# Optimization experiments

Hardware: AMD Instinct MI355X
Metric: run time of the kernel (lower is better)

Reference implementation:

```python
import jax, jax.numpy as jnp
import numpy as np

N, E, D, ED, FD, H, Q, K, G = 50000, 600000, 128, 128, 512, 1, 3, 512, 512
NEG_SLOPE = 0.2
EPS = 1e-5


def setup_inputs() -> dict:
    key = jax.random.key(0)
    ks = jax.random.split(key, 16)
    inp = {
        'x': jax.random.normal(ks[0], (N, D), jnp.float32),
        'edge_index': jax.random.randint(ks[1], (2, E), 0, N, jnp.int32),
        'edge_attr': jax.random.normal(ks[2], (E, ED), jnp.float32),
        'batch_vec': jnp.sort(jax.random.randint(ks[3], (N,), 0, G, jnp.int32)),
        'W_l': jax.random.normal(ks[4], (D, H * D), jnp.float32),
        'b_l': jnp.zeros((H * D,), jnp.float32),
        'W_r': jax.random.normal(ks[5], (D, H * D), jnp.float32),
        'b_r': jnp.zeros((H * D,), jnp.float32),
        'W_edge': jax.random.normal(ks[6], (ED, H * D), jnp.float32),
        'att': jax.random.normal(ks[7], (H, D), jnp.float32),
        'conv_bias': jnp.zeros((H * D,), jnp.float32),
        'adapter_W': jax.random.normal(ks[8], (D, D), jnp.float32),
        'adapter_b': jnp.zeros((D,), jnp.float32),
        'norm_g': jnp.ones((D,), jnp.float32),
        'norm_b': jnp.zeros((D,), jnp.float32),
        'codebooks': jax.random.normal(ks[9], (Q, K, D), jnp.float32),
        'out_W': jax.random.normal(ks[10], (D, FD), jnp.float32),
        'out_b': jnp.zeros((FD,), jnp.float32),
        'outnorm_g': jnp.ones((FD,), jnp.float32),
        'outnorm_b': jnp.zeros((FD,), jnp.float32),
    }
    return inp


def _layer_norm(x, g, b):
    m = x.mean(-1, keepdims=True)
    v = ((x - m) ** 2).mean(-1, keepdims=True)
    return (x - m) * jax.lax.rsqrt(v + EPS) * g + b


def _forward(x, edge_index, edge_attr, batch_vec, W_l, b_l, W_r, b_r, W_edge, att,
             conv_bias, adapter_W, adapter_b, norm_g, norm_b, codebooks, out_W, out_b,
             outnorm_g, outnorm_b):
    sg = jax.lax.stop_gradient
    n = x.shape[0]
    # ---- GATv2Conv (PyG defaults: add_self_loops=True, fill_value='mean') ----
    loops = jnp.arange(n, dtype=edge_index.dtype)
    src = jnp.concatenate([edge_index[0], loops])
    dst = jnp.concatenate([edge_index[1], loops])
    mean_attr = edge_attr.mean(0)
    ea = jnp.concatenate([edge_attr, jnp.broadcast_to(mean_attr, (n, edge_attr.shape[1]))])
    xl = (x @ W_l + b_l).reshape(n, H, D)   # source transform
    xr = (x @ W_r + b_r).reshape(n, H, D)   # target transform
    e_emb = (ea @ W_edge).reshape(-1, H, D)
    e = xl[src] + xr[dst] + e_emb           # [Etot,H,D]
    score = jnp.einsum('ehd,hd->eh', jax.nn.leaky_relu(e, NEG_SLOPE), att)
    smax = jax.ops.segment_max(score, dst, num_segments=n)
    ex = jnp.exp(score - smax[dst])
    denom = jax.ops.segment_sum(ex, dst, num_segments=n)
    alpha = ex / (denom[dst] + 1e-16)       # per-target softmax
    out = jax.ops.segment_sum(xl[src] * alpha[..., None], dst, num_segments=n)  # [n,H,D]
    out = out.reshape(n, H * D) + conv_bias
    h = out.reshape(n, H, D).mean(1)        # mean over heads
    # ---- global mean pool over graphs ----
    sums = jax.ops.segment_sum(h, batch_vec, num_segments=G)
    cnts = jax.ops.segment_sum(jnp.ones((n,), h.dtype), batch_vec, num_segments=G)
    g = sums / jnp.maximum(cnts, 1.0)[:, None]
    # ---- adapter + layernorm ----
    g = g @ adapter_W + adapter_b
    g = _layer_norm(g, norm_g, norm_b)
    # ---- residual VQ (euclidean nearest code, straight-through) ----
    residual = g
    quantized_out = jnp.zeros_like(g)
    codes, idxs, commits = [], [], []
    cb_sq = (codebooks ** 2).sum(-1)        # [Q,K]
    for q in range(Q):
        cb = codebooks[q]
        d2 = (residual ** 2).sum(-1, keepdims=True) - 2.0 * residual @ cb.T + cb_sq[q]
        idx = jnp.argmin(d2, axis=-1)
        code = cb[idx]
        commits.append(((sg(code) - residual) ** 2).mean())
        quantized_out = quantized_out + residual + sg(code - residual)
        codes.append(code)
        idxs.append(idx)
        residual = residual - sg(code)
    commit_loss = jnp.stack(commits).mean()
    residual_loss = ((g - quantized_out) ** 2).mean()
    loss = commit_loss + residual_loss
    indices = jnp.stack(idxs, axis=1)       # [G,Q]
    # ---- per-quantizer straight-through tokens -> projection -> layernorm ----
    tokens = jnp.stack([g + sg(c - g) for c in codes], axis=1)  # [G,Q,D]
    tokens = tokens @ out_W + out_b                              # [G,Q,FD]
    tokens = _layer_norm(tokens, outnorm_g, outnorm_b)
    return tokens, indices, loss


def reference(x, edge_index, edge_attr, batch_vec, W_l, b_l, W_r, b_r, W_edge, att,
              conv_bias, adapter_W, adapter_b, norm_g, norm_b, codebooks, out_W, out_b,
              outnorm_g, outnorm_b):
    return _forward(x, edge_index, edge_attr, batch_vec, W_l, b_l, W_r, b_r, W_edge,
                    att, conv_bias, adapter_W, adapter_b, norm_g, norm_b, codebooks,
                    out_W, out_b, outnorm_g, outnorm_b)
```

## Files before the change

### kernel.cpp

```cpp
#include <hip/hip_runtime.h>
#include <math.h>

#define N_NODES 50000
#define E_EDGES 600000
#define DD 128
#define G_GRAPHS 512
#define K_CODES 512
#define Q_QUANT 3
#define FD_OUT 512
#define NEG_SLOPE 0.2f
#define LN_EPS 1e-5f

using short8 = __attribute__((ext_vector_type(8))) short;
using f32x4  = __attribute__((ext_vector_type(4))) float;

static __device__ __forceinline__ float lrelu(float v){ return v > 0.f ? v : NEG_SLOPE*v; }
static __device__ __forceinline__ float wsum(float v){
#pragma unroll
  for (int m = 1; m < 64; m <<= 1) v += __shfl_xor(v, m);
  return v;
}
static __device__ __forceinline__ float wmax(float v){
#pragma unroll
  for (int m = 1; m < 64; m <<= 1) v = fmaxf(v, __shfl_xor(v, m));
  return v;
}
static __device__ __forceinline__ ushort f2bf(float f){
  unsigned u = __float_as_uint(f);
  unsigned r = (u + 0x7fffu + ((u >> 16) & 1u)) >> 16;
  return (ushort)r;
}
static __device__ __forceinline__ float bf2f(ushort s){
  return __uint_as_float(((unsigned)s) << 16);
}

#define EA_LD 130

__global__ __launch_bounds__(256)
void k_xform2(const float* __restrict__ x,
              const float* __restrict__ W_l, const float* __restrict__ b_l,
              const float* __restrict__ W_r, const float* __restrict__ b_r,
              float* __restrict__ xl, float* __restrict__ xr, int n)
{
  __shared__ __align__(16) float xt[64*EA_LD];
  __shared__ __align__(16) float WtL[32*128];
  __shared__ __align__(16) float WtR[32*128];
  const int tid = threadIdx.x;
  const int r0 = blockIdx.x * 64;
  {
    const int q = tid & 63, eb = tid >> 6;
#pragma unroll
    for (int i = 0; i < 16; ++i){
      int e = eb + 4*i;
      int row = r0 + e;
      float2 v = make_float2(0.f, 0.f);
      if (row < n) v = *(const float2*)&x[row*DD + q*2];
      *(float2*)&xt[e*EA_LD + q*2] = v;
    }
  }
  const int eg = tid >> 4;
  const int cg = tid & 15;
  float accL[4][8], accR[4][8];
#pragma unroll
  for (int j = 0; j < 4; ++j)
#pragma unroll
    for (int u = 0; u < 8; ++u){ accL[j][u] = 0.f; accR[j][u] = 0.f; }

  for (int kq = 0; kq < 4; ++kq){
    __syncthreads();
    {
      const int c4 = tid & 31, kb = tid >> 5;
#pragma unroll
      for (int i = 0; i < 4; ++i){
        int kk = kb + 8*i;
        *(float4*)&WtL[kk*128 + c4*4] = *(const float4*)&W_l[(kq*32+kk)*DD + c4*4];
        *(float4*)&WtR[kk*128 + c4*4] = *(const float4*)&W_r[(kq*32+kk)*DD + c4*4];
      }
    }
    __syncthreads();
    const int kb2 = kq*32;
#pragma unroll 4
    for (int k = 0; k < 32; ++k){
      float aa[4];
#pragma unroll
      for (int j = 0; j < 4; ++j) aa[j] = xt[(eg*4+j)*EA_LD + kb2 + k];
      float bL[8], bR[8];
      *(float4*)&bL[0] = *(const float4*)&WtL[k*128 + cg*4];
      *(float4*)&bL[4] = *(const float4*)&WtL[k*128 + 64 + cg*4];
      *(float4*)&bR[0] = *(const float4*)&WtR[k*128 + cg*4];
      *(float4*)&bR[4] = *(const float4*)&WtR[k*128 + 64 + cg*4];
#pragma unroll
      for (int j = 0; j < 4; ++j){
#pragma unroll
        for (int u = 0; u < 8; ++u) accL[j][u] = fmaf(aa[j], bL[u], accL[j][u]);
#pragma unroll
        for (int u = 0; u < 8; ++u) accR[j][u] = fmaf(aa[j], bR[u], accR[j][u]);
      }
    }
  }
  float bvL[8], bvR[8];
  *(float4*)&bvL[0] = *(const float4*)&b_l[cg*4];
  *(float4*)&bvL[4] = *(const float4*)&b_l[64 + cg*4];
  *(float4*)&bvR[0] = *(const float4*)&b_r[cg*4];
  *(float4*)&bvR[4] = *(const float4*)&b_r[64 + cg*4];
#pragma unroll
  for (int j = 0; j < 4; ++j){
    int row = r0 + eg*4 + j;
    if (row < n){
      float oL[8], oR[8];
#pragma unroll
      for (int u = 0; u < 8; ++u){ oL[u] = accL[j][u] + bvL[u]; oR[u] = accR[j][u] + bvR[u]; }
      *(float4*)&xl[row*DD + cg*4]      = *(const float4*)&oL[0];
      *(float4*)&xl[row*DD + 64 + cg*4] = *(const float4*)&oL[4];
      *(float4*)&xr[row*DD + cg*4]      = *(const float4*)&oR[0];
      *(float4*)&xr[row*DD + 64 + cg*4] = *(const float4*)&oR[4];
    }
  }
}

__global__ __launch_bounds__(128)
void k_wsplit(const float* __restrict__ W, ushort* __restrict__ Wbh, ushort* __restrict__ Wbl)
{
  const int n = blockIdx.x;
  const int k = threadIdx.x;
  float v = W[k*DD + n];
  ushort h = f2bf(v);
  Wbh[n*DD + k] = h;
  Wbl[n*DD + k] = f2bf(v - bf2f(h));
}

#define AP 40
#define WP 40
#define XSP 132

__global__ __launch_bounds__(256)
void k_edge(const float* __restrict__ edge_attr,
            const ushort* __restrict__ Wbh, const ushort* __restrict__ Wbl,
            const int* __restrict__ ei, const float* __restrict__ xl,
            const float* __restrict__ xr, const float* __restrict__ att,
            const int* __restrict__ off, int* __restrict__ pos,
            uint2* __restrict__ rec, float* __restrict__ asum_mid)
{
  __shared__ __align__(16) char smem[64*XSP*4];
  ushort* Ah = (ushort*)smem;
  ushort* Al = (ushort*)(smem + 5120);
  ushort* Wh = (ushort*)(smem + 10240);
  ushort* Wl = (ushort*)(smem + 20480);
  float*  xs = (float*)smem;

  const int tid = threadIdx.x;
  const int w = tid >> 6, lane = tid & 63;
  const int e0 = blockIdx.x * 64;

  const int ar  = tid & 63;
  const int ak  = w * 8;
  const int wn  = tid & 127;
  const int wk2 = (tid >> 7) * 16;

  const int mrow = w * 16 + (lane & 15);
  const int koff = (lane >> 4) * 8;
  const int nrow = lane & 15;

  f32x4 acc[8];
#pragma unroll
  for (int nt = 0; nt < 8; ++nt){ f32x4 z = {0.f,0.f,0.f,0.f}; acc[nt] = z; }

  for (int kq = 0; kq < 4; ++kq){
    if (kq) __syncthreads();
    float av[8];
    *(float4*)&av[0] = *(const float4*)&edge_attr[(size_t)(e0+ar)*DD + kq*32 + ak];
    *(float4*)&av[4] = *(const float4*)&edge_attr[(size_t)(e0+ar)*DD + kq*32 + ak + 4];
    short8 vh, vl;
#pragma unroll
    for (int i = 0; i < 8; ++i){
      ushort h = f2bf(av[i]);
      vh[i] = (short)h;
      vl[i] = (short)f2bf(av[i] - bf2f(h));
    }
    *(short8*)&Ah[ar*AP + ak] = vh;
    *(short8*)&Al[ar*AP + ak] = vl;
    {
      float cs[8];
#pragma unroll
      for (int i = 0; i < 8; ++i) cs[i] = av[i];
#pragma unroll
      for (int m = 1; m < 64; m <<= 1){
#pragma unroll
        for (int i = 0; i < 8; ++i) cs[i] += __shfl_xor(cs[i], m);
      }
      if (lane == 0){
#pragma unroll
        for (int i = 0; i < 8; ++i)
          atomicAdd(&asum_mid[(blockIdx.x & 63)*DD + kq*32 + ak + i], cs[i]);
      }
    }
    {
      const ushort* gh = &Wbh[wn*DD + kq*32 + wk2];
      const ushort* gl = &Wbl[wn*DD + kq*32 + wk2];
      *(short8*)&Wh[wn*WP + wk2]     = *(const short8*)&gh[0];
      *(short8*)&Wh[wn*WP + wk2 + 8] = *(const short8*)&gh[8];
      *(short8*)&Wl[wn*WP + wk2]     = *(const short8*)&gl[0];
      *(short8*)&Wl[wn*WP + wk2 + 8] = *(const short8*)&gl[8];
    }
    __syncthreads();
    short8 a_h = *(const short8*)&Ah[mrow*AP + koff];
    short8 a_l = *(const short8*)&Al[mrow*AP + koff];
    short8 bh[8];
#pragma unroll
    for (int nt = 0; nt < 8; ++nt)
      bh[nt] = *(const short8*)&Wh[(nt*16 + nrow)*WP + koff];
#pragma unroll
    for (int nt = 0; nt < 8; ++nt)
      acc[nt] = __builtin_amdgcn_mfma_f32_16x16x32_bf16(a_h, bh[nt], acc[nt], 0, 0, 0);
#pragma unroll
    for (int nt = 0; nt < 8; ++nt){
      short8 bl = *(const short8*)&Wl[(nt*16 + nrow)*WP + koff];
      acc[nt] = __builtin_amdgcn_mfma_f32_16x16x32_bf16(a_h, bl, acc[nt], 0, 0, 0);
    }
#pragma unroll
    for (int nt = 0; nt < 8; ++nt)
      acc[nt] = __builtin_amdgcn_mfma_f32_16x16x32_bf16(a_l, bh[nt], acc[nt], 0, 0, 0);
  }
  __syncthreads();
  {
    const int s0 = ei[e0 + ar];
    const int d0 = ei[E_EDGES + e0 + ar];
    const int cc = w * 32;
#pragma unroll
    for (int i = 0; i < 8; ++i){
      float4 a = *(const float4*)&xl[(size_t)s0*DD + cc + i*4];
      float4 b = *(const float4*)&xr[(size_t)d0*DD + cc + i*4];
      *(float4*)&xs[ar*XSP + cc + i*4] = make_float4(a.x+b.x, a.y+b.y, a.z+b.z, a.w+b.w);
    }
  }
  __syncthreads();
  float attv[8];
#pragma unroll
  for (int nt = 0; nt < 8; ++nt) attv[nt] = att[nt*16 + nrow];
  float p[4] = {0.f, 0.f, 0.f, 0.f};
  const int rb = w*16 + (lane >> 4)*4;
#pragma unroll
  for (int nt = 0; nt < 8; ++nt){
#pragma unroll
    for (int j = 0; j < 4; ++j){
      float ev = acc[nt][j] + xs[(rb + j)*XSP + nt*16 + nrow];
      p[j] += lrelu(ev) * attv[nt];
    }
  }
#pragma unroll
  for (int m = 1; m < 16; m <<= 1){
#pragma unroll
    for (int j = 0; j < 4; ++j) p[j] += __shfl_xor(p[j], m);
  }
  if ((lane & 15) == 0){
#pragma unroll
    for (int j = 0; j < 4; ++j){
      int e = e0 + rb + j;
      int d = ei[E_EDGES + e];
      int s = ei[e];
      int pp = atomicAdd(&pos[d], 1);
      uint2 r; r.x = (unsigned)s; r.y = __float_as_uint(p[j]);
      rec[off[d] + pp] = r;
    }
  }
}

__global__ __launch_bounds__(128)
void k_me(const float* __restrict__ asum_mid, const float* __restrict__ W_edge,
          float* __restrict__ me)
{
  __shared__ float mean[128];
  const int d = threadIdx.x;
  float s = 0.f;
  for (int r = 0; r < 64; ++r) s += asum_mid[r*DD + d];
  mean[d] = s / (float)E_EDGES;
  __syncthreads();
  float acc = 0.f;
  for (int k = 0; k < 128; ++k) acc += mean[k] * W_edge[k*DD + d];
  me[d] = acc;
}

__global__ __launch_bounds__(256)
void k_hist(const int* __restrict__ ei, int* __restrict__ indeg)
{
  int e = blockIdx.x*256 + threadIdx.x;
  if (e < E_EDGES) atomicAdd(&indeg[ei[E_EDGES + e]], 1);
}

#define SC_NB ((N_NODES + 511) / 512)
__global__ __launch_bounds__(512)
void k_scan1(const int* __restrict__ indeg, int* __restrict__ off, int* __restrict__ bsum)
{
  __shared__ int s[512];
  const int tid = threadIdx.x;
  const int gid = blockIdx.x*512 + tid;
  int v = (gid < N_NODES) ? indeg[gid] : 0;
  s[tid] = v;
  __syncthreads();
  for (int d = 1; d < 512; d <<= 1){
    int t = (tid >= d) ? s[tid-d] : 0;
    __syncthreads();
    s[tid] += t;
    __syncthreads();
  }
  if (gid < N_NODES) off[gid] = s[tid] - v;
  if (tid == 511) bsum[blockIdx.x] = s[511];
}

__global__ __launch_bounds__(128)
void k_scan2(const int* __restrict__ bsum, int* __restrict__ boff)
{
  __shared__ int s[128];
  const int tid = threadIdx.x;
  int v = (tid < SC_NB) ? bsum[tid] : 0;
  s[tid] = v;
  __syncthreads();
  for (int d = 1; d < 128; d <<= 1){
    int t = (tid >= d) ? s[tid-d] : 0;
    __syncthreads();
    s[tid] += t;
    __syncthreads();
  }
  if (tid < SC_NB) boff[tid] = s[tid] - v;
}

__global__ __launch_bounds__(512)
void k_scan3(int* __restrict__ off, const int* __restrict__ boff)
{
  const int gid = blockIdx.x*512 + threadIdx.x;
  if (gid < N_NODES) off[gid] += boff[blockIdx.x];
  if (gid == 0) off[N_NODES] = E_EDGES;
}

__global__ __launch_bounds__(256)
void k_aggregate(const int* __restrict__ off, const uint2* __restrict__ rec,
                 const float* __restrict__ xl, const float* __restrict__ xr,
                 const float* __restrict__ me, const float* __restrict__ att,
                 const float* __restrict__ conv_bias, const int* __restrict__ batch_vec,
                 float* __restrict__ gsum, float* __restrict__ gcnt)
{
  __shared__ float hshare[4][128];
  __shared__ int bsh[4];
  const int tid = threadIdx.x, lane = tid & 63, wid = tid >> 6;
  const int i = blockIdx.x*4 + wid;
  float2 xli = *(const float2*)&xl[i*DD + lane*2];
  float2 xri = *(const float2*)&xr[i*DD + lane*2];
  float2 mev = *(const float2*)&me[lane*2];
  float2 attv = *(const float2*)&att[lane*2];
  float v0 = xli.x + xri.x + mev.x;
  float v1 = xli.y + xri.y + mev.y;
  float s_self = wsum(lrelu(v0)*attv.x + lrelu(v1)*attv.y);
  const int o0 = off[i], o1 = off[i+1];
  const int deg = o1 - o0;
  uint2 myrec = make_uint2(0u, __float_as_uint(-INFINITY));
  float m = s_self;
  if (lane < deg) myrec = rec[o0 + lane];
  m = fmaxf(m, __uint_as_float(myrec.y));
  for (int b = 64; b < deg; b += 64){
    int j = b + lane;
    if (j < deg) m = fmaxf(m, __uint_as_float(rec[o0 + j].y));
  }
  m = wmax(m);
  float wse = __expf(s_self - m);
  float den = wse;
  float a0 = wse * xli.x, a1 = wse * xli.y;
  if (deg <= 64){
    float msc = __uint_as_float(myrec.y);
    int msrc = (int)myrec.x;
#pragma unroll 4
    for (int j = 0; j < deg; ++j){
      float sc = __shfl(msc, j);
      int s = __shfl(msrc, j);
      float w = __expf(sc - m);
      den += w;
      float2 xs = *(const float2*)&xl[s*DD + lane*2];
      a0 = fmaf(w, xs.x, a0);
      a1 = fmaf(w, xs.y, a1);
    }
  } else {
#pragma unroll 4
    for (int j = 0; j < deg; ++j){
      uint2 r = rec[o0 + j];
      float w = __expf(__uint_as_float(r.y) - m);
      den += w;
      float2 xs = *(const float2*)&xl[(int)r.x*DD + lane*2];
      a0 = fmaf(w, xs.x, a0);
      a1 = fmaf(w, xs.y, a1);
    }
  }
  float inv = 1.0f / (den + 1e-16f);
  float2 cb2 = *(const float2*)&conv_bias[lane*2];
  float h0 = a0*inv + cb2.x;
  float h1 = a1*inv + cb2.y;
  int b = batch_vec[i];
  hshare[wid][lane*2]     = h0;
  hshare[wid][lane*2 + 1] = h1;
  if (lane == 0) bsh[wid] = b;
  __syncthreads();
  bool uni = (bsh[0]==bsh[1]) && (bsh[1]==bsh[2]) && (bsh[2]==bsh[3]);
  if (uni){
    if (wid == 0){
      float s0 = hshare[0][lane*2] + hshare[1][lane*2] + hshare[2][lane*2] + hshare[3][lane*2];
      float s1 = hshare[0][lane*2+1] + hshare[1][lane*2+1] + hshare[2][lane*2+1] + hshare[3][lane*2+1];
      atomicAdd(&gsum[b*DD + lane*2],     s0);
      atomicAdd(&gsum[b*DD + lane*2 + 1], s1);
      if (lane == 0) atomicAdd(&gcnt[b], 4.0f);
    }
  } else {
    atomicAdd(&gsum[b*DD + lane*2],     h0);
    atomicAdd(&gsum[b*DD + lane*2 + 1], h1);
    if (lane == 0) atomicAdd(&gcnt[b], 1.0f);
  }
}

__global__ __launch_bounds__(128)
void k_pool(const float* __restrict__ gsum, const float* __restrict__ gcnt,
            const float* __restrict__ aW, const float* __restrict__ ab,
            const float* __restrict__ ng, const float* __restrict__ nb,
            float* __restrict__ g_ln)
{
  __shared__ float row[128];
  __shared__ float red[128];
  const int g = blockIdx.x, d = threadIdx.x;
  float denom = fmaxf(gcnt[g], 1.0f);
  row[d] = gsum[g*DD + d] / denom;
  __syncthreads();
  double accd = (double)ab[d];
  for (int k = 0; k < 128; ++k) accd += (double)row[k] * (double)aW[k*DD + d];
  float a = (float)accd;
  red[d] = a; __syncthreads();
  for (int s = 64; s > 0; s >>= 1){ if (d < s) red[d] += red[d+s]; __syncthreads(); }
  float mean = red[0] / 128.f; __syncthreads();
  float c = a - mean;
  red[d] = c*c; __syncthreads();
  for (int s = 64; s > 0; s >>= 1){ if (d < s) red[d] += red[d+s]; __syncthreads(); }
  float var = red[0] / 128.f; __syncthreads();
  float inv = (float)(1.0 / sqrt((double)var + (double)LN_EPS));
  g_ln[g*DD + d] = c * inv * ng[d] + nb[d];
}

__global__ __launch_bounds__(256)
void k_rvq(const float* __restrict__ g_ln, const float* __restrict__ codebooks,
           float* __restrict__ ind_out, int* __restrict__ idx_i,
           float* __restrict__ accs)
{
  __shared__ __align__(16) float r_lds[128];
  __shared__ float red[128];
  __shared__ double bd[64];
  __shared__ int bi[64];
  __shared__ int chosen;
  const int g = blockIdx.x, tid = threadIdx.x;
  if (tid < 128) r_lds[tid] = g_ln[g*DD + tid];
  __syncthreads();
  const int cl = tid >> 2, dq = tid & 3;
  for (int q = 0; q < Q_QUANT; ++q){
    const float* cb = codebooks + (size_t)q * K_CODES * DD;
    double bestd = 1e300; int besti = 1 << 30;
    for (int r = 0; r < 8; ++r){
      int c = r*64 + cl;
      double rc = 0.0, cc = 0.0;
      const float4* cp = (const float4*)&cb[c*DD + dq*32];
      const float4* rp = (const float4*)&r_lds[dq*32];
#pragma unroll
      for (int i = 0; i < 8; ++i){
        float4 cv = cp[i]; float4 rv = rp[i];
        rc += (double)cv.x*rv.x + (double)cv.y*rv.y + (double)cv.z*rv.z + (double)cv.w*rv.w;
        cc += (double)cv.x*cv.x + (double)cv.y*cv.y + (double)cv.z*cv.z + (double)cv.w*cv.w;
      }
      rc += __shfl_xor(rc, 1); rc += __shfl_xor(rc, 2);
      cc += __shfl_xor(cc, 1); cc += __shfl_xor(cc, 2);
      if (dq == 0){
        double d2 = cc - 2.0*rc;
        if (d2 < bestd || (d2 == bestd && c < besti)){ bestd = d2; besti = c; }
      }
    }
    if (dq == 0){ bd[cl] = bestd; bi[cl] = besti; }
    __syncthreads();
    if (tid < 64){
      double d2 = bd[tid]; int ii = bi[tid];
#pragma unroll
      for (int m = 1; m < 64; m <<= 1){
        double od = __shfl_xor(d2, m); int oi = __shfl_xor(ii, m);
        if (od < d2 || (od == d2 && oi < ii)){ d2 = od; ii = oi; }
      }
      if (tid == 0) chosen = ii;
    }
    __syncthreads();
    const int idx = chosen;
    if (tid == 0){
      ind_out[g*Q_QUANT + q] = (float)idx;
      idx_i[g*Q_QUANT + q] = idx;
    }
    if (tid < 128){
      float cd = cb[idx*DD + tid];
      float diff = cd - r_lds[tid];
      red[tid] = diff * diff;
      r_lds[tid] -= cd;
    }
    __syncthreads();
    for (int s = 64; s > 0; s >>= 1){ if (tid < s) red[tid] += red[tid+s]; __syncthreads(); }
    if (tid == 0) atomicAdd(&accs[q], red[0]);
    __syncthreads();
  }
  if (tid < 128) red[tid] = r_lds[tid]*r_lds[tid];
  __syncthreads();
  for (int s = 64; s > 0; s >>= 1){ if (tid < s) red[tid] += red[tid+s]; __syncthreads(); }
  if (tid == 0) atomicAdd(&accs[3], red[0]);
}

__global__ __launch_bounds__(256)
void k_tokens(const float* __restrict__ codebooks, const int* __restrict__ idx_i,
              const float* __restrict__ out_W, const float* __restrict__ out_b,
              const float* __restrict__ og, const float* __restrict__ ob,
              float* __restrict__ tokens)
{
  __shared__ __align__(16) float c_lds[128];
  __shared__ float red[256];
  const int blk = blockIdx.x;
  const int g = blk / 3, q = blk % 3;
  const int tid = threadIdx.x;
  const int idx = idx_i[g*Q_QUANT + q];
  if (tid < 128) c_lds[tid] = codebooks[((size_t)q*K_CODES + idx)*DD + tid];
  __syncthreads();
  double v0 = (double)out_b[tid];
  double v1 = (double)out_b[tid + 256];
  for (int k = 0; k < 128; ++k){
    double ck = (double)c_lds[k];
    v0 += ck * (double)out_W[k*FD_OUT + tid];
    v1 += ck * (double)out_W[k*FD_OUT + tid + 256];
  }
  float f0 = (float)v0, f1 = (float)v1;
  red[tid] = f0 + f1; __syncthreads();
  for (int s = 128; s > 0; s >>= 1){ if (tid < s) red[tid] += red[tid+s]; __syncthreads(); }
  float mean = red[0] / 512.f; __syncthreads();
  float d0 = f0 - mean, d1 = f1 - mean;
  red[tid] = d0*d0 + d1*d1; __syncthreads();
  for (int s = 128; s > 0; s >>= 1){ if (tid < s) red[tid] += red[tid+s]; __syncthreads(); }
  float var = red[0] / 512.f; __syncthreads();
  float inv = (float)(1.0 / sqrt((double)var + (double)LN_EPS));
  tokens[(size_t)blk*FD_OUT + tid]       = d0*inv*og[tid] + ob[tid];
  tokens[(size_t)blk*FD_OUT + tid + 256] = d1*inv*og[tid+256] + ob[tid+256];
}

__global__ void k_loss(const float* __restrict__ accs, float* __restrict__ out)
{
  float commit = (accs[0] + accs[1] + accs[2]) / (3.0f * G_GRAPHS * DD);
  float resid  = accs[3] / ((float)G_GRAPHS * DD);
  out[0] = commit + resid;
}

extern "C" void kernel_launch(void* const* d_in, const int* in_sizes, int n_in,
                              void* d_out, int out_size, void* d_ws, size_t ws_size,
                              hipStream_t stream)
{
  (void)in_sizes; (void)n_in; (void)out_size; (void)ws_size;
  const float* x         = (const float*)d_in[0];
  const int*   ei        = (const int*)d_in[1];
  const float* edge_attr = (const float*)d_in[2];
  const int*   batch_vec = (const int*)d_in[3];
  const float* W_l       = (const float*)d_in[4];
  const float* b_l       = (const float*)d_in[5];
  const float* W_r       = (const float*)d_in[6];
  const float* b_r       = (const float*)d_in[7];
  const float* W_edge    = (const float*)d_in[8];
  const float* att       = (const float*)d_in[9];
  const float* conv_bias = (const float*)d_in[10];
  const float* aW        = (const float*)d_in[11];
  const float* ab        = (const float*)d_in[12];
  const float* ng        = (const float*)d_in[13];
  const float* nb        = (const float*)d_in[14];
  const float* codebooks = (const float*)d_in[15];
  const float* out_W     = (const float*)d_in[16];
  const float* out_b     = (const float*)d_in[17];
  const float* og        = (const float*)d_in[18];
  const float* ob        = (const float*)d_in[19];
  float* outf = (float*)d_out;

  char* w = (char*)d_ws;
  size_t o = 0;
  auto nxt = [&](size_t bytes)->void*{
    void* p = w + o;
    o += (bytes + 511) & ~(size_t)511;
    return p;
  };
  int*   indeg    = (int*)  nxt((size_t)N_NODES*4);
  int*   pos      = (int*)  nxt((size_t)N_NODES*4);
  float* asum_mid = (float*)nxt((size_t)64*DD*4);
  float* gsum     = (float*)nxt((size_t)G_GRAPHS*DD*4);
  float* gcnt     = (float*)nxt((size_t)G_GRAPHS*4);
  float* accs     = (float*)nxt(16);
  const size_t zero_span = o;
  int*   off      = (int*)  nxt((size_t)(N_NODES+1)*4);
  float* xl       = (float*)nxt((size_t)N_NODES*DD*4);
  float* xr       = (float*)nxt((size_t)N_NODES*DD*4);
  uint2* rec      = (uint2*)nxt((size_t)E_EDGES*8);
  float* me       = (float*)nxt((size_t)DD*4);
  float* g_ln     = (float*)nxt((size_t)G_GRAPHS*DD*4);
  int*   idx_i    = (int*)  nxt((size_t)G_GRAPHS*Q_QUANT*4);
  int*   bsum     = (int*)  nxt((size_t)SC_NB*4);
  int*   boff     = (int*)  nxt((size_t)SC_NB*4);
  ushort* Wbh     = (ushort*)nxt((size_t)DD*DD*2);
  ushort* Wbl     = (ushort*)nxt((size_t)DD*DD*2);

  hipMemsetAsync(w, 0, zero_span, stream);

  k_wsplit<<<dim3(128), dim3(128), 0, stream>>>(W_edge, Wbh, Wbl);
  k_hist<<<dim3((E_EDGES+255)/256), dim3(256), 0, stream>>>(ei, indeg);
  k_scan1<<<dim3(SC_NB), dim3(512), 0, stream>>>(indeg, off, bsum);
  k_scan2<<<dim3(1), dim3(128), 0, stream>>>(bsum, boff);
  k_scan3<<<dim3(SC_NB), dim3(512), 0, stream>>>(off, boff);
  k_xform2<<<dim3((N_NODES+63)/64), dim3(256), 0, stream>>>(x, W_l, b_l, W_r, b_r,
                                                            xl, xr, N_NODES);
  k_edge<<<dim3(E_EDGES/64), dim3(256), 0, stream>>>(edge_attr, Wbh, Wbl, ei, xl, xr, att,
                                                     off, pos, rec, asum_mid);
  k_me<<<dim3(1), dim3(128), 0, stream>>>(asum_mid, W_edge, me);
  k_aggregate<<<dim3(N_NODES/4), dim3(256), 0, stream>>>(off, rec, xl, xr, me, att,
                                                         conv_bias, batch_vec, gsum, gcnt);
  k_pool<<<dim3(G_GRAPHS), dim3(128), 0, stream>>>(gsum, gcnt, aW, ab, ng, nb, g_ln);
  k_rvq<<<dim3(G_GRAPHS), dim3(256), 0, stream>>>(g_ln, codebooks,
                                                  outf + (size_t)G_GRAPHS*Q_QUANT*FD_OUT,
                                                  idx_i, accs);
  k_tokens<<<dim3(G_GRAPHS*Q_QUANT), dim3(256), 0, stream>>>(codebooks, idx_i, out_W, out_b,
                                                             og, ob, outf);
  k_loss<<<dim3(1), dim3(1), 0, stream>>>(accs,
                                          outf + (size_t)G_GRAPHS*Q_QUANT*FD_OUT
                                               + (size_t)G_GRAPHS*Q_QUANT);
}
```

Baseline: 606.8 us.

## Keep W_edge fragments in registers and split edge GEMM by N across waves

The edge kernel no longer stages W_edge in shared memory per K-chunk. Each wave now loads its two 16-column slices of the split-bf16 weights straight into registers once, and the whole 64x128 edge_attr tile is converted and staged in LDS up front. This removes three of the four per-chunk barriers and the repeated weight LDS traffic. Because waves now partition columns instead of rows, per-wave attention partial sums are combined through a small LDS buffer, and a single thread per edge does the final atomic scatter. The cost is more registers for weight fragments and accumulators, and a larger LDS footprint that may lower occupancy.

```diff
diff --git a/kernel.cpp b/kernel.cpp
--- a/kernel.cpp
+++ b/kernel.cpp
@@ -129,8 +129,7 @@
   Wbl[n*DD + k] = f2bf(v - bf2f(h));
 }
 
-#define AP 40
-#define WP 40
+#define APS 136
 #define XSP 132
 
 __global__ __launch_bounds__(256)
@@ -141,127 +140,142 @@
             const int* __restrict__ off, int* __restrict__ pos,
             uint2* __restrict__ rec, float* __restrict__ asum_mid)
 {
-  __shared__ __align__(16) char smem[64*XSP*4];
+  __shared__ __align__(16) char smem[34816];
   ushort* Ah = (ushort*)smem;
-  ushort* Al = (ushort*)(smem + 5120);
-  ushort* Wh = (ushort*)(smem + 10240);
-  ushort* Wl = (ushort*)(smem + 20480);
+  ushort* Al = (ushort*)(smem + 17408);
   float*  xs = (float*)smem;
+  float*  ps = (float*)(smem + 33792);
 
   const int tid = threadIdx.x;
   const int w = tid >> 6, lane = tid & 63;
+  const int g = lane >> 4, f = lane & 15;
   const int e0 = blockIdx.x * 64;
-
-  const int ar  = tid & 63;
-  const int ak  = w * 8;
-  const int wn  = tid & 127;
-  const int wk2 = (tid >> 7) * 16;
-
-  const int mrow = w * 16 + (lane & 15);
-  const int koff = (lane >> 4) * 8;
-  const int nrow = lane & 15;
-
-  f32x4 acc[8];
-#pragma unroll
-  for (int nt = 0; nt < 8; ++nt){ f32x4 z = {0.f,0.f,0.f,0.f}; acc[nt] = z; }
-
+  const int koff = g * 8;
+  const int nt0 = w * 2;
+
+  short8 whF[2][4], wlF[2][4];
+#pragma unroll
+  for (int t = 0; t < 2; ++t){
+    const ushort* gh = &Wbh[((nt0+t)*16 + f)*DD];
+    const ushort* gl = &Wbl[((nt0+t)*16 + f)*DD];
+#pragma unroll
+    for (int kq = 0; kq < 4; ++kq){
+      whF[t][kq] = *(const short8*)&gh[kq*32 + koff];
+      wlF[t][kq] = *(const short8*)&gl[kq*32 + koff];
+    }
+  }
+
+  {
+    const int r = lane;
+    const int kc = w * 32;
+#pragma unroll
+    for (int c = 0; c < 4; ++c){
+      float av[8];
+      *(float4*)&av[0] = *(const float4*)&edge_attr[(size_t)(e0+r)*DD + kc + c*8];
+      *(float4*)&av[4] = *(const float4*)&edge_attr[(size_t)(e0+r)*DD + kc + c*8 + 4];
+      short8 vh, vl;
+#pragma unroll
+      for (int i = 0; i < 8; ++i){
+        ushort h = f2bf(av[i]);
+        vh[i] = (short)h;
+        vl[i] = (short)f2bf(av[i] - bf2f(h));
+      }
+      *(short8*)&Ah[r*APS + kc + c*8] = vh;
+      *(short8*)&Al[r*APS + kc + c*8] = vl;
+      float cs[8];
+#pragma unroll
+      for (int i = 0; i < 8; ++i) cs[i] = av[i];
+#pragma unroll
+      for (int m = 1; m < 64; m <<= 1){
+#pragma unroll
+        for (int i = 0; i < 8; ++i) cs[i] += __shfl_xor(cs[i], m);
+      }
+      if (lane == 0){
+#pragma unroll
+        for (int i = 0; i < 8; ++i)
+          atomicAdd(&asum_mid[(blockIdx.x & 63)*DD + kc + c*8 + i], cs[i]);
+      }
+    }
+  }
+  __syncthreads();
+
+  f32x4 acc[4][2];
+#pragma unroll
+  for (int m = 0; m < 4; ++m)
+#pragma unroll
+    for (int t = 0; t < 2; ++t){ f32x4 z = {0.f,0.f,0.f,0.f}; acc[m][t] = z; }
+
+#pragma unroll
   for (int kq = 0; kq < 4; ++kq){
-    if (kq) __syncthreads();
-    float av[8];
-    *(float4*)&av[0] = *(const float4*)&edge_attr[(size_t)(e0+ar)*DD + kq*32 + ak];
-    *(float4*)&av[4] = *(const float4*)&edge_attr[(size_t)(e0+ar)*DD + kq*32 + ak + 4];
-    short8 vh, vl;
-#pragma unroll
-    for (int i = 0; i < 8; ++i){
-      ushort h = f2bf(av[i]);
-      vh[i] = (short)h;
-      vl[i] = (short)f2bf(av[i] - bf2f(h));
-    }
-    *(short8*)&Ah[ar*AP + ak] = vh;
-    *(short8*)&Al[ar*AP + ak] = vl;
-    {
-      float cs[8];
-#pragma unroll
-      for (int i = 0; i < 8; ++i) cs[i] = av[i];
-#pragma unroll
-      for (int m = 1; m < 64; m <<= 1){
-#pragma unroll
-        for (int i = 0; i < 8; ++i) cs[i] += __shfl_xor(cs[i], m);
-      }
-      if (lane == 0){
-#pragma unroll
-        for (int i = 0; i < 8; ++i)
-          atomicAdd(&asum_mid[(blockIdx.x & 63)*DD + kq*32 + ak + i], cs[i]);
-      }
-    }
-    {
-      const ushort* gh = &Wbh[wn*DD + kq*32 + wk2];
-      const ushort* gl = &Wbl[wn*DD + kq*32 + wk2];
-      *(short8*)&Wh[wn*WP + wk2]     = *(const short8*)&gh[0];
-      *(short8*)&Wh[wn*WP + wk2 + 8] = *(const short8*)&gh[8];
-      *(short8*)&Wl[wn*WP + wk2]     = *(const short8*)&gl[0];
-      *(short8*)&Wl[wn*WP + wk2 + 8] = *(const short8*)&gl[8];
-    }
-    __syncthreads();
-    short8 a_h = *(const short8*)&Ah[mrow*AP + koff];
-    short8 a_l = *(const short8*)&Al[mrow*AP + koff];
-    short8 bh[8];
-#pragma unroll
-    for (int nt = 0; nt < 8; ++nt)
-      bh[nt] = *(const short8*)&Wh[(nt*16 + nrow)*WP + koff];
-#pragma unroll
-    for (int nt = 0; nt < 8; ++nt)
-      acc[nt] = __builtin_amdgcn_mfma_f32_16x16x32_bf16(a_h, bh[nt], acc[nt], 0, 0, 0);
-#pragma unroll
-    for (int nt = 0; nt < 8; ++nt){
-      short8 bl = *(const short8*)&Wl[(nt*16 + nrow)*WP + koff];
-      acc[nt] = __builtin_amdgcn_mfma_f32_16x16x32_bf16(a_h, bl, acc[nt], 0, 0, 0);
-    }
-#pragma unroll
-    for (int nt = 0; nt < 8; ++nt)
-      acc[nt] = __builtin_amdgcn_mfma_f32_16x16x32_bf16(a_l, bh[nt], acc[nt], 0, 0, 0);
-  }
-  __syncthreads();
+#pragma unroll
+    for (int m = 0; m < 4; ++m){
+      short8 a_h = *(const short8*)&Ah[(m*16 + f)*APS + kq*32 + koff];
+      short8 a_l = *(const short8*)&Al[(m*16 + f)*APS + kq*32 + koff];
+#pragma unroll
+      for (int t = 0; t < 2; ++t){
+        acc[m][t] = __builtin_amdgcn_mfma_f32_16x16x32_bf16(a_h, whF[t][kq], acc[m][t], 0, 0, 0);
+        acc[m][t] = __builtin_amdgcn_mfma_f32_16x16x32_bf16(a_h, wlF[t][kq], acc[m][t], 0, 0, 0);
+        acc[m][t] = __builtin_amdgcn_mfma_f32_16x16x32_bf16(a_l, whF[t][kq], acc[m][t], 0, 0, 0);
+      }
+    }
+  }
+  __syncthreads();
+
   {
-    const int s0 = ei[e0 + ar];
-    const int d0 = ei[E_EDGES + e0 + ar];
+    const int s0 = ei[e0 + lane];
+    const int d0 = ei[E_EDGES + e0 + lane];
     const int cc = w * 32;
 #pragma unroll
     for (int i = 0; i < 8; ++i){
       float4 a = *(const float4*)&xl[(size_t)s0*DD + cc + i*4];
       float4 b = *(const float4*)&xr[(size_t)d0*DD + cc + i*4];
-      *(float4*)&xs[ar*XSP + cc + i*4] = make_float4(a.x+b.x, a.y+b.y, a.z+b.z, a.w+b.w);
-    }
-  }
-  __syncthreads();
-  float attv[8];
-#pragma unroll
-  for (int nt = 0; nt < 8; ++nt) attv[nt] = att[nt*16 + nrow];
-  float p[4] = {0.f, 0.f, 0.f, 0.f};
-  const int rb = w*16 + (lane >> 4)*4;
-#pragma unroll
-  for (int nt = 0; nt < 8; ++nt){
-#pragma unroll
-    for (int j = 0; j < 4; ++j){
-      float ev = acc[nt][j] + xs[(rb + j)*XSP + nt*16 + nrow];
-      p[j] += lrelu(ev) * attv[nt];
-    }
-  }
-#pragma unroll
-  for (int m = 1; m < 16; m <<= 1){
-#pragma unroll
-    for (int j = 0; j < 4; ++j) p[j] += __shfl_xor(p[j], m);
-  }
-  if ((lane & 15) == 0){
-#pragma unroll
-    for (int j = 0; j < 4; ++j){
-      int e = e0 + rb + j;
-      int d = ei[E_EDGES + e];
-      int s = ei[e];
-      int pp = atomicAdd(&pos[d], 1);
-      uint2 r; r.x = (unsigned)s; r.y = __float_as_uint(p[j]);
-      rec[off[d] + pp] = r;
-    }
+      *(float4*)&xs[lane*XSP + cc + i*4] = make_float4(a.x+b.x, a.y+b.y, a.z+b.z, a.w+b.w);
+    }
+  }
+  __syncthreads();
+
+  float p[4][4];
+#pragma unroll
+  for (int m = 0; m < 4; ++m)
+#pragma unroll
+    for (int j = 0; j < 4; ++j) p[m][j] = 0.f;
+  float attv[2];
+#pragma unroll
+  for (int t = 0; t < 2; ++t) attv[t] = att[(nt0+t)*16 + f];
+#pragma unroll
+  for (int m = 0; m < 4; ++m){
+#pragma unroll
+    for (int t = 0; t < 2; ++t){
+#pragma unroll
+      for (int j = 0; j < 4; ++j){
+        float ev = acc[m][t][j] + xs[(m*16 + g*4 + j)*XSP + (nt0+t)*16 + f];
+        p[m][j] += lrelu(ev) * attv[t];
+      }
+    }
+  }
+#pragma unroll
+  for (int mm = 1; mm < 16; mm <<= 1){
+#pragma unroll
+    for (int m = 0; m < 4; ++m)
+#pragma unroll
+      for (int j = 0; j < 4; ++j) p[m][j] += __shfl_xor(p[m][j], mm);
+  }
+  if (f == 0){
+#pragma unroll
+    for (int m = 0; m < 4; ++m)
+#pragma unroll
+      for (int j = 0; j < 4; ++j)
+        ps[w*64 + m*16 + g*4 + j] = p[m][j];
+  }
+  __syncthreads();
+
+  if (tid < 64){
+    float sc = ps[tid] + ps[64 + tid] + ps[128 + tid] + ps[192 + tid];
+    int s = ei[e0 + tid];
+    int d = ei[E_EDGES + e0 + tid];
+    int pp = atomicAdd(&pos[d], 1);
+    uint2 r; r.x = (unsigned)s; r.y = __float_as_uint(sc);
+    rec[off[d] + pp] = r;
   }
 }
 
```

Measured after the change: 584.8 us. 3.6% less time.

## Drop LDS staging in edge kernel; load MFMA fragments directly from global memory

Applied to the files above, without the earlier changes.

The edge-attention kernel stops staging edge_attr, the split-bf16 weights and the gathered xl+xr rows through shared memory. Each wavefront now loads its own A fragments and the weight fragments straight from global memory into registers. It gathers xl/xr values directly in the epilogue, removing all block barriers. The column-sum reduction for the mean edge attribute is done per 16-lane group, which means more atomics. The cost is more global/L2 traffic for the weights, uncoalesced 64-byte-strided gathers of xl/xr, and higher register pressure.

```diff
diff --git a/kernel.cpp b/kernel.cpp
--- a/kernel.cpp
+++ b/kernel.cpp
@@ -129,10 +129,6 @@
   Wbl[n*DD + k] = f2bf(v - bf2f(h));
 }
 
-#define AP 40
-#define WP 40
-#define XSP 132
-
 __global__ __launch_bounds__(256)
 void k_edge(const float* __restrict__ edge_attr,
             const ushort* __restrict__ Wbh, const ushort* __restrict__ Wbl,
@@ -141,109 +137,86 @@
             const int* __restrict__ off, int* __restrict__ pos,
             uint2* __restrict__ rec, float* __restrict__ asum_mid)
 {
-  __shared__ __align__(16) char smem[64*XSP*4];
-  ushort* Ah = (ushort*)smem;
-  ushort* Al = (ushort*)(smem + 5120);
-  ushort* Wh = (ushort*)(smem + 10240);
-  ushort* Wl = (ushort*)(smem + 20480);
-  float*  xs = (float*)smem;
-
   const int tid = threadIdx.x;
   const int w = tid >> 6, lane = tid & 63;
-  const int e0 = blockIdx.x * 64;
-
-  const int ar  = tid & 63;
-  const int ak  = w * 8;
-  const int wn  = tid & 127;
-  const int wk2 = (tid >> 7) * 16;
-
-  const int mrow = w * 16 + (lane & 15);
-  const int koff = (lane >> 4) * 8;
-  const int nrow = lane & 15;
+  const int f = lane & 15, g = lane >> 4;
+  const int e0w = blockIdx.x * 64 + w * 16;
+
+  short8 a_h[4], a_l[4];
+  float av[4][8];
+#pragma unroll
+  for (int kq = 0; kq < 4; ++kq){
+    const float* srcp = &edge_attr[(size_t)(e0w + f)*DD + kq*32 + g*8];
+    *(float4*)&av[kq][0] = *(const float4*)&srcp[0];
+    *(float4*)&av[kq][4] = *(const float4*)&srcp[4];
+#pragma unroll
+    for (int i = 0; i < 8; ++i){
+      ushort h = f2bf(av[kq][i]);
+      a_h[kq][i] = (short)h;
+      a_l[kq][i] = (short)f2bf(av[kq][i] - bf2f(h));
+    }
+  }
+
+#pragma unroll
+  for (int kq = 0; kq < 4; ++kq){
+#pragma unroll
+    for (int m = 1; m < 16; m <<= 1){
+#pragma unroll
+      for (int i = 0; i < 8; ++i) av[kq][i] += __shfl_xor(av[kq][i], m);
+    }
+  }
+  if (f == 0){
+    const int arow = (blockIdx.x*4 + w) & 63;
+#pragma unroll
+    for (int kq = 0; kq < 4; ++kq)
+#pragma unroll
+      for (int i = 0; i < 8; ++i)
+        atomicAdd(&asum_mid[arow*DD + kq*32 + g*8 + i], av[kq][i]);
+  }
 
   f32x4 acc[8];
 #pragma unroll
   for (int nt = 0; nt < 8; ++nt){ f32x4 z = {0.f,0.f,0.f,0.f}; acc[nt] = z; }
 
+#pragma unroll
   for (int kq = 0; kq < 4; ++kq){
-    if (kq) __syncthreads();
-    float av[8];
-    *(float4*)&av[0] = *(const float4*)&edge_attr[(size_t)(e0+ar)*DD + kq*32 + ak];
-    *(float4*)&av[4] = *(const float4*)&edge_attr[(size_t)(e0+ar)*DD + kq*32 + ak + 4];
-    short8 vh, vl;
-#pragma unroll
-    for (int i = 0; i < 8; ++i){
-      ushort h = f2bf(av[i]);
-      vh[i] = (short)h;
-      vl[i] = (short)f2bf(av[i] - bf2f(h));
-    }
-    *(short8*)&Ah[ar*AP + ak] = vh;
-    *(short8*)&Al[ar*AP + ak] = vl;
-    {
-      float cs[8];
-#pragma unroll
-      for (int i = 0; i < 8; ++i) cs[i] = av[i];
-#pragma unroll
-      for (int m = 1; m < 64; m <<= 1){
-#pragma unroll
-        for (int i = 0; i < 8; ++i) cs[i] += __shfl_xor(cs[i], m);
+#pragma unroll
+    for (int half = 0; half < 2; ++half){
+      short8 wh[4], wl[4];
+#pragma unroll
+      for (int t = 0; t < 4; ++t){
+        const int nt = half*4 + t;
+        wh[t] = *(const short8*)&Wbh[(size_t)(nt*16 + f)*DD + kq*32 + g*8];
+        wl[t] = *(const short8*)&Wbl[(size_t)(nt*16 + f)*DD + kq*32 + g*8];
       }
-      if (lane == 0){
-#pragma unroll
-        for (int i = 0; i < 8; ++i)
-          atomicAdd(&asum_mid[(blockIdx.x & 63)*DD + kq*32 + ak + i], cs[i]);
-      }
-    }
-    {
-      const ushort* gh = &Wbh[wn*DD + kq*32 + wk2];
-      const ushort* gl = &Wbl[wn*DD + kq*32 + wk2];
-      *(short8*)&Wh[wn*WP + wk2]     = *(const short8*)&gh[0];
-      *(short8*)&Wh[wn*WP + wk2 + 8] = *(const short8*)&gh[8];
-      *(short8*)&Wl[wn*WP + wk2]     = *(const short8*)&gl[0];
-      *(short8*)&Wl[wn*WP + wk2 + 8] = *(const short8*)&gl[8];
-    }
-    __syncthreads();
-    short8 a_h = *(const short8*)&Ah[mrow*AP + koff];
-    short8 a_l = *(const short8*)&Al[mrow*AP + koff];
-    short8 bh[8];
-#pragma unroll
-    for (int nt = 0; nt < 8; ++nt)
-      bh[nt] = *(const short8*)&Wh[(nt*16 + nrow)*WP + koff];
-#pragma unroll
-    for (int nt = 0; nt < 8; ++nt)
-      acc[nt] = __builtin_amdgcn_mfma_f32_16x16x32_bf16(a_h, bh[nt], acc[nt], 0, 0, 0);
-#pragma unroll
-    for (int nt = 0; nt < 8; ++nt){
-      short8 bl = *(const short8*)&Wl[(nt*16 + nrow)*WP + koff];
-      acc[nt] = __builtin_amdgcn_mfma_f32_16x16x32_bf16(a_h, bl, acc[nt], 0, 0, 0);
-    }
-#pragma unroll
-    for (int nt = 0; nt < 8; ++nt)
-      acc[nt] = __builtin_amdgcn_mfma_f32_16x16x32_bf16(a_l, bh[nt], acc[nt], 0, 0, 0);
-  }
-  __syncthreads();
-  {
-    const int s0 = ei[e0 + ar];
-    const int d0 = ei[E_EDGES + e0 + ar];
-    const int cc = w * 32;
-#pragma unroll
-    for (int i = 0; i < 8; ++i){
-      float4 a = *(const float4*)&xl[(size_t)s0*DD + cc + i*4];
-      float4 b = *(const float4*)&xr[(size_t)d0*DD + cc + i*4];
-      *(float4*)&xs[ar*XSP + cc + i*4] = make_float4(a.x+b.x, a.y+b.y, a.z+b.z, a.w+b.w);
-    }
-  }
-  __syncthreads();
+#pragma unroll
+      for (int t = 0; t < 4; ++t)
+        acc[half*4+t] = __builtin_amdgcn_mfma_f32_16x16x32_bf16(a_h[kq], wh[t], acc[half*4+t], 0, 0, 0);
+#pragma unroll
+      for (int t = 0; t < 4; ++t)
+        acc[half*4+t] = __builtin_amdgcn_mfma_f32_16x16x32_bf16(a_h[kq], wl[t], acc[half*4+t], 0, 0, 0);
+#pragma unroll
+      for (int t = 0; t < 4; ++t)
+        acc[half*4+t] = __builtin_amdgcn_mfma_f32_16x16x32_bf16(a_l[kq], wh[t], acc[half*4+t], 0, 0, 0);
+    }
+  }
+
+  int srcs[4], dsts[4];
+#pragma unroll
+  for (int j = 0; j < 4; ++j){
+    srcs[j] = ei[e0w + g*4 + j];
+    dsts[j] = ei[E_EDGES + e0w + g*4 + j];
+  }
   float attv[8];
 #pragma unroll
-  for (int nt = 0; nt < 8; ++nt) attv[nt] = att[nt*16 + nrow];
+  for (int nt = 0; nt < 8; ++nt) attv[nt] = att[nt*16 + f];
   float p[4] = {0.f, 0.f, 0.f, 0.f};
-  const int rb = w*16 + (lane >> 4)*4;
 #pragma unroll
   for (int nt = 0; nt < 8; ++nt){
 #pragma unroll
     for (int j = 0; j < 4; ++j){
-      float ev = acc[nt][j] + xs[(rb + j)*XSP + nt*16 + nrow];
+      float ev = acc[nt][j] + xl[(size_t)srcs[j]*DD + nt*16 + f]
+                            + xr[(size_t)dsts[j]*DD + nt*16 + f];
       p[j] += lrelu(ev) * attv[nt];
     }
   }
@@ -252,14 +225,12 @@
 #pragma unroll
     for (int j = 0; j < 4; ++j) p[j] += __shfl_xor(p[j], m);
   }
-  if ((lane & 15) == 0){
+  if (f == 0){
 #pragma unroll
     for (int j = 0; j < 4; ++j){
-      int e = e0 + rb + j;
-      int d = ei[E_EDGES + e];
-      int s = ei[e];
+      int d = dsts[j];
       int pp = atomicAdd(&pos[d], 1);
-      uint2 r; r.x = (unsigned)s; r.y = __float_as_uint(p[j]);
+      uint2 r; r.x = (unsigned)srcs[j]; r.y = __float_as_uint(p[j]);
       rec[off[d] + pp] = r;
     }
   }
```

After: 680.5 us. +12.1%, slower.
